# Kernel optimization log

Measured on AMD Instinct MI355X. Metric: run time of the kernel, lower is better.

Reference implementation:

```python
import jax, jax.numpy as jnp
import numpy as np

B, N, C, E = 8, 4096, 128, 131072  # batch, nodes, channels (in==out), edges


def _linear_params(key, fan_in, fan_out):
    kw, kb = jax.random.split(key)
    s = 1.0 / np.sqrt(fan_in).astype(np.float32)
    W = jax.random.uniform(kw, (fan_in, fan_out), jnp.float32, -s, s)
    b = jax.random.uniform(kb, (fan_out,), jnp.float32, -s, s)
    return W, b


def setup_inputs() -> dict:
    key = jax.random.key(0)
    ks = jax.random.split(key, 6)
    x = jax.random.normal(ks[0], (B, N, C), jnp.float32)
    edge_index = jax.random.randint(ks[1], (2, E), 0, N, jnp.int64)
    W0, b0 = _linear_params(ks[2], C, C)        # lin0: in -> out
    W1, b1 = _linear_params(ks[3], 2 * C, C)    # lin1: 2*out -> out
    W2, b2 = _linear_params(ks[4], C, C)        # lin2: out -> out
    Wo, bo = _linear_params(ks[5], C, C)        # output: out -> out
    return {"x": x, "edge_index": edge_index, "W0": W0, "b0": b0,
            "W1": W1, "b1": b1, "W2": W2, "b2": b2, "Wo": Wo, "bo": bo}


def reference(x, edge_index, W0, b0, W1, b1, W2, b2, Wo, bo):
    n = x.shape[1]
    # symmetric 0/1 adjacency (duplicate edges collapse via .set), zero diagonal
    adj = jnp.zeros((n, n), x.dtype)
    adj = adj.at[edge_index[0], edge_index[1]].set(1.0)
    adj = adj.at[edge_index[1], edge_index[0]].set(1.0)
    diag = jnp.arange(n)
    adj = adj.at[diag, diag].set(0.0)
    h = x @ W0 + b0                               # [B, N, C]
    agg = jnp.einsum('ij,bjd->bid', adj, h)       # neighbor aggregation
    cat = jnp.concatenate([x, agg], axis=-1)      # [B, N, 2C]
    out = (cat @ W1 + b1) @ W2 + b2
    out = jax.nn.gelu(out, approximate=False) @ Wo + bo  # torch exact GELU
    return x + out
```

## Files before the change

### kernel.cpp

```cpp
#include <hip/hip_runtime.h>
#include <hip/hip_bf16.h>
#include <math.h>

#define NN 4096
#define BB 8
#define CC 128
#define EE 131072
#define M_ROWS (BB*NN)
#define DEG_CAP 512

typedef __attribute__((ext_vector_type(8))) short short8;
typedef __attribute__((ext_vector_type(4))) float f32x4;

__device__ __forceinline__ float bf2f(unsigned int u){
    union { unsigned int i; float f; } v; v.i = u << 16; return v.f;
}
__device__ __forceinline__ unsigned short f2bf(float f){
    union { float f; unsigned int i; } v; v.f = f;
    unsigned int u = v.i;
    unsigned int r = u + 0x7FFFu + ((u >> 16) & 1u);
    return (unsigned short)(r >> 16);
}

__device__ __forceinline__ int swz(int r, int k2 ){
    return r * 256 + (k2 ^ ((r & 7) << 4));
}

__global__ __launch_bounds__(256) void k_init(uint4* __restrict__ bits4,
                                              const float* __restrict__ x,
                                              unsigned short* __restrict__ xb,
                                              const float* __restrict__ W0, const float* __restrict__ W1,
                                              const float* __restrict__ W2, const float* __restrict__ Wo,
                                              unsigned short* __restrict__ Wt1a, unsigned short* __restrict__ Wt1b,
                                              unsigned short* __restrict__ Wt2,  unsigned short* __restrict__ Wto,
                                              unsigned short* __restrict__ W0bf){
    int bid = blockIdx.x, t = threadIdx.x;
    if (bid < 512){
        bits4[bid * 256 + t] = (uint4){0u, 0u, 0u, 0u};
        return;
    }
    if (bid < 2560){
        size_t e = (size_t)(bid - 512) * 2048 + t * 8;
        float4 lo = *((const float4*)(x + e));
        float4 hi = *((const float4*)(x + e + 4));
        ushort4 w0, w1;
        w0.x = f2bf(lo.x); w0.y = f2bf(lo.y); w0.z = f2bf(lo.z); w0.w = f2bf(lo.w);
        w1.x = f2bf(hi.x); w1.y = f2bf(hi.y); w1.z = f2bf(hi.z); w1.w = f2bf(hi.w);
        *((ushort4*)(xb + e)) = w0;
        *((ushort4*)(xb + e + 4)) = w1;
        return;
    }
    int idx = (bid - 2560) * 256 + t;
    int s = idx >> 14;
    int e = idx & 16383;
    int n = e >> 7, k = e & 127;
    float v; unsigned short* dst;
    switch (s){
        case 0:  v = W1[k*128+n];        dst = Wt1a; break;
        case 1:  v = W1[(128+k)*128+n];  dst = Wt1b; break;
        case 2:  v = W2[k*128+n];        dst = Wt2;  break;
        case 3:  v = Wo[k*128+n];        dst = Wto;  break;
        default: v = W0[n*128+k];        dst = W0bf; break;
    }
    dst[n*128+k] = f2bf(v);
}

__global__ __launch_bounds__(256) void k_scatter(const int* __restrict__ ei,
                                                 unsigned int* __restrict__ bits){
    int e = blockIdx.x * blockDim.x + threadIdx.x;
    if (e < EE){
        int u = ei[e], v = ei[EE + e];
        atomicOr(&bits[u * 128 + (v >> 5)], 1u << (v & 31));
        atomicOr(&bits[v * 128 + (u >> 5)], 1u << (u & 31));
    }
}

__global__ __launch_bounds__(128) void k_csr(const unsigned int* __restrict__ bits,
                                             int* __restrict__ cols, int* __restrict__ deg){
    __shared__ int sc[128];
    int i = blockIdx.x, t = threadIdx.x;
    unsigned int w = bits[i * 128 + t];
    if (t == (i >> 5)) w &= ~(1u << (i & 31));
    int c = __popc(w);
    sc[t] = c; __syncthreads();
    int val = c;
    for (int off = 1; off < 128; off <<= 1){
        int add = (t >= off) ? sc[t - off] : 0;
        __syncthreads();
        val += add; sc[t] = val;
        __syncthreads();
    }
    int total = sc[127];
    int pos = val - c;
    unsigned int ww = w;
    while (ww){
        int b = __ffs(ww) - 1;
        ww &= ww - 1;
        if (pos < DEG_CAP) cols[(size_t)i * DEG_CAP + pos] = t * 32 + b;
        pos++;
    }
    if (t == 0) deg[i] = total < DEG_CAP ? total : DEG_CAP;
}

__device__ __forceinline__ void stage_w(const unsigned short* __restrict__ Wt,
                                        unsigned short* Ws, int t){
    #pragma unroll
    for (int it = 0; it < 8; ++it){
        int g = it * 2048 + t * 8;
        int r = g >> 7, k = g & 127;
        uint4 v = *((const uint4*)(Wt + r * 128 + k));
        *((uint4*)((char*)Ws + swz(r, k * 2))) = v;
    }
}
__device__ __forceinline__ void stage_a_bf16(const unsigned short* __restrict__ src, int blockRow,
                                             unsigned short* As, int t){
    #pragma unroll
    for (int it = 0; it < 4; ++it){
        int g = it * 2048 + t * 8;
        int r = g >> 7, k = g & 127;
        uint4 v = *((const uint4*)(src + (size_t)(blockRow + r) * 128 + k));
        *((uint4*)((char*)As + swz(r, k * 2))) = v;
    }
}
__device__ __forceinline__ void mfma_pass(const unsigned short* As, const unsigned short* Ws,
                                          int wr, int wc, int l15, int lh, f32x4 acc[2][4]){
    #pragma unroll
    for (int ks = 0; ks < 4; ++ks){
        const int kc = ks * 32 + lh * 8;
        short8 af[2], bfv[4];
        #pragma unroll
        for (int m = 0; m < 2; m++){
            int r = wr + m * 16 + l15;
            af[m] = *((const short8*)((const char*)As + swz(r, kc * 2)));
        }
        #pragma unroll
        for (int n = 0; n < 4; n++){
            int r = wc + n * 16 + l15;
            bfv[n] = *((const short8*)((const char*)Ws + swz(r, kc * 2)));
        }
        #pragma unroll
        for (int m = 0; m < 2; m++)
            #pragma unroll
            for (int n = 0; n < 4; n++)
                acc[m][n] = __builtin_amdgcn_mfma_f32_16x16x32_bf16(af[m], bfv[n], acc[m][n], 0, 0, 0);
    }
}

__global__ __launch_bounds__(256) void k_wprod(const unsigned short* __restrict__ W0bf,
                                               const unsigned short* __restrict__ Wt1b,
                                               const float* __restrict__ b0,
                                               const float* __restrict__ W1,
                                               unsigned short* __restrict__ Wtu,
                                               float* __restrict__ c1){
    __shared__ unsigned short As[128*128];
    __shared__ unsigned short Ws[128*128];
    const int t = threadIdx.x;
    stage_w(W0bf, As, t);
    stage_w(Wt1b, Ws, t);
    __syncthreads();
    const int lane = t & 63, w = t >> 6;
    const int wr = w * 32;
    const int l15 = lane & 15, lh = lane >> 4;
    f32x4 acc[2][8];
    #pragma unroll
    for (int m = 0; m < 2; m++) for (int n = 0; n < 8; n++) acc[m][n] = (f32x4)(0.0f);
    #pragma unroll
    for (int ks = 0; ks < 4; ++ks){
        const int kc = ks * 32 + lh * 8;
        short8 af[2], bfv[8];
        #pragma unroll
        for (int m = 0; m < 2; m++){
            int r = wr + m * 16 + l15;
            af[m] = *((const short8*)((const char*)As + swz(r, kc * 2)));
        }
        #pragma unroll
        for (int n = 0; n < 8; n++){
            int r = n * 16 + l15;
            bfv[n] = *((const short8*)((const char*)Ws + swz(r, kc * 2)));
        }
        #pragma unroll
        for (int m = 0; m < 2; m++)
            #pragma unroll
            for (int n = 0; n < 8; n++)
                acc[m][n] = __builtin_amdgcn_mfma_f32_16x16x32_bf16(af[m], bfv[n], acc[m][n], 0, 0, 0);
    }
    #pragma unroll
    for (int m = 0; m < 2; m++){
        #pragma unroll
        for (int rr = 0; rr < 4; rr++){
            int r = wr + m * 16 + lh * 4 + rr;
            #pragma unroll
            for (int n = 0; n < 8; n++){
                int c = n * 16 + l15;
                Wtu[c * 128 + r] = f2bf(acc[m][n][rr]);
            }
        }
    }
    if (t < 128){
        float s = 0.f;
        #pragma unroll 8
        for (int k = 0; k < 128; k++)
            s += b0[k] * W1[(size_t)(128 + k) * 128 + t];
        c1[t] = s;
    }
}

__device__ __forceinline__ void acc8u(uint4 u, float* a){
    a[0] += bf2f(u.x & 0xFFFFu); a[1] += bf2f(u.x >> 16);
    a[2] += bf2f(u.y & 0xFFFFu); a[3] += bf2f(u.y >> 16);
    a[4] += bf2f(u.z & 0xFFFFu); a[5] += bf2f(u.z >> 16);
    a[6] += bf2f(u.w & 0xFFFFu); a[7] += bf2f(u.w >> 16);
}

__global__ __launch_bounds__(256) void k_agg(const unsigned short* __restrict__ h,
                                             const int* __restrict__ cols,
                                             const int* __restrict__ deg,
                                             unsigned short* __restrict__ agg){
    __shared__ int scol[4][DEG_CAP];
    const int t = threadIdx.x;
    const int w = t >> 6, lane = t & 63;
    const int sub = lane >> 4, li = lane & 15;
    const int b = blockIdx.x & 7;
    const int i = ((blockIdx.x >> 3) << 2) + w;
    const int d = deg[i];
    const int* cl = cols + (size_t)i * DEG_CAP;
    for (int q = lane; q < d; q += 64) scol[w][q] = cl[q];

    const unsigned short* hb = h + (size_t)b * (NN*128) + li * 8;
    float a[8];
    #pragma unroll
    for (int c = 0; c < 8; c++) a[c] = 0.f;

    int n = sub;
    for (; n + 4 < d; n += 8){
        int j0 = scol[w][n], j1 = scol[w][n+4];
        uint4 u0 = *((const uint4*)(hb + ((size_t)j0 << 7)));
        uint4 u1 = *((const uint4*)(hb + ((size_t)j1 << 7)));
        acc8u(u0, a); acc8u(u1, a);
    }
    if (n < d){
        uint4 u0 = *((const uint4*)(hb + ((size_t)scol[w][n] << 7)));
        acc8u(u0, a);
    }
    #pragma unroll
    for (int c = 0; c < 8; c++){
        a[c] += __shfl_xor(a[c], 16);
        a[c] += __shfl_xor(a[c], 32);
    }
    if (sub == 0){
        uint4 o;
        o.x = (unsigned)f2bf(a[0]) | ((unsigned)f2bf(a[1]) << 16);
        o.y = (unsigned)f2bf(a[2]) | ((unsigned)f2bf(a[3]) << 16);
        o.z = (unsigned)f2bf(a[4]) | ((unsigned)f2bf(a[5]) << 16);
        o.w = (unsigned)f2bf(a[6]) | ((unsigned)f2bf(a[7]) << 16);
        *((uint4*)(agg + (size_t)b * (NN*128) + ((size_t)i << 7) + li * 8)) = o;
    }
}

__global__ __launch_bounds__(256) void k_mlp(const unsigned short* __restrict__ xb,
                                             const unsigned short* __restrict__ u,
                                             const unsigned short* __restrict__ Wt1a,
                                             const unsigned short* __restrict__ Wtu,
                                             const unsigned short* __restrict__ Wt2,
                                             const unsigned short* __restrict__ Wto,
                                             const float* __restrict__ c1,
                                             const float* __restrict__ b1,
                                             const float* __restrict__ b2,
                                             const float* __restrict__ bo,
                                             const int* __restrict__ deg,
                                             const float* __restrict__ x,
                                             float* __restrict__ out){
    __shared__ unsigned short As[64*128];
    __shared__ unsigned short Ws[128*128];
    const int t = threadIdx.x;
    const int blockRow = blockIdx.x * 64;
    const int lane = t & 63, w = t >> 6;
    const int wr = (w >> 1) * 32, wc = (w & 1) * 64;
    const int l15 = lane & 15, lh = lane >> 4;

    f32x4 acc[2][4];
    #pragma unroll
    for (int m = 0; m < 2; m++) for (int n = 0; n < 4; n++) acc[m][n] = (f32x4)(0.0f);

    stage_a_bf16(xb, blockRow, As, t);
    stage_w(Wt1a, Ws, t);
    __syncthreads();
    mfma_pass(As, Ws, wr, wc, l15, lh, acc);
    __syncthreads();
    stage_a_bf16(u, blockRow, As, t);
    stage_w(Wtu, Ws, t);
    __syncthreads();
    mfma_pass(As, Ws, wr, wc, l15, lh, acc);
    __syncthreads();

    #pragma unroll
    for (int m = 0; m < 2; m++){
        #pragma unroll
        for (int rr = 0; rr < 4; rr++){
            int rl = wr + m * 16 + lh * 4 + rr;
            int node = (blockRow + rl) & (NN - 1);
            float degf = (float)deg[node];
            #pragma unroll
            for (int n = 0; n < 4; n++){
                int col = wc + n * 16 + l15;
                float v = acc[m][n][rr] + b1[col] + degf * c1[col];
                *((unsigned short*)((char*)As + swz(rl, col * 2))) = f2bf(v);
            }
        }
    }
    stage_w(Wt2, Ws, t);
    __syncthreads();

    f32x4 acc2[2][4];
    #pragma unroll
    for (int m = 0; m < 2; m++) for (int n = 0; n < 4; n++) acc2[m][n] = (f32x4)(0.0f);
    mfma_pass(As, Ws, wr, wc, l15, lh, acc2);
    __syncthreads();

    #pragma unroll
    for (int m = 0; m < 2; m++){
        #pragma unroll
        for (int rr = 0; rr < 4; rr++){
            int rl = wr + m * 16 + lh * 4 + rr;
            #pragma unroll
            for (int n = 0; n < 4; n++){
                int col = wc + n * 16 + l15;
                float v = acc2[m][n][rr] + b2[col];
                v = 0.5f * v * (1.0f + erff(v * 0.70710678118f));
                *((unsigned short*)((char*)As + swz(rl, col * 2))) = f2bf(v);
            }
        }
    }
    stage_w(Wto, Ws, t);
    __syncthreads();

    f32x4 acc3[2][4];
    #pragma unroll
    for (int m = 0; m < 2; m++) for (int n = 0; n < 4; n++) acc3[m][n] = (f32x4)(0.0f);
    mfma_pass(As, Ws, wr, wc, l15, lh, acc3);

    #pragma unroll
    for (int m = 0; m < 2; m++){
        #pragma unroll
        for (int rr = 0; rr < 4; rr++){
            int row = blockRow + wr + m * 16 + lh * 4 + rr;
            #pragma unroll
            for (int n = 0; n < 4; n++){
                int col = wc + n * 16 + l15;
                float v = acc3[m][n][rr] + bo[col] + x[(size_t)row * 128 + col];
                out[(size_t)row * 128 + col] = v;
            }
        }
    }
}

extern "C" void kernel_launch(void* const* d_in, const int* in_sizes, int n_in,
                              void* d_out, int out_size, void* d_ws, size_t ws_size,
                              hipStream_t stream) {
    const float* x  = (const float*)d_in[0];
    const int*   ei = (const int*)d_in[1];
    const float* W0 = (const float*)d_in[2];
    const float* b0 = (const float*)d_in[3];
    const float* W1 = (const float*)d_in[4];
    const float* b1 = (const float*)d_in[5];
    const float* W2 = (const float*)d_in[6];
    const float* b2 = (const float*)d_in[7];
    const float* Wo = (const float*)d_in[8];
    const float* bo = (const float*)d_in[9];
    float* out = (float*)d_out;

    char* ws = (char*)d_ws;
    unsigned int* bits   = (unsigned int*)(ws + 0);
    int*   cols          = (int*)(ws + 2097152);
    int*   deg           = (int*)(ws + 10485760);
    unsigned short* xb   = (unsigned short*)(ws + 10502144);
    unsigned short* ubuf = (unsigned short*)(ws + 18890752);
    unsigned short* Wt1a = (unsigned short*)(ws + 27279360);
    unsigned short* Wt1b = (unsigned short*)(ws + 27279360 + 32768);
    unsigned short* Wt2  = (unsigned short*)(ws + 27279360 + 65536);
    unsigned short* Wto  = (unsigned short*)(ws + 27279360 + 98304);
    unsigned short* W0bf = (unsigned short*)(ws + 27279360 + 131072);
    unsigned short* Wtu  = (unsigned short*)(ws + 27279360 + 163840);
    float* c1            = (float*)(ws + 27279360 + 196608);

    k_init<<<2880, 256, 0, stream>>>((uint4*)bits, x, xb, W0, W1, W2, Wo,
                                     Wt1a, Wt1b, Wt2, Wto, W0bf);
    k_scatter<<<EE / 256, 256, 0, stream>>>(ei, bits);
    k_csr<<<NN, 128, 0, stream>>>(bits, cols, deg);
    k_wprod<<<1, 256, 0, stream>>>(W0bf, Wt1b, b0, W1, Wtu, c1);
    k_agg<<<BB * (NN / 4), 256, 0, stream>>>(xb, cols, deg, ubuf);
    k_mlp<<<M_ROWS / 64, 256, 0, stream>>>(xb, ubuf, Wt1a, Wtu, Wt2, Wto,
                                           c1, b1, b2, bo, deg, x, out);
}
```

Before: 77.13 us.

## Fuse weight-product into scatter kernel, shrink CSR cols to u16, residual from bf16 tile

Result: no change. 77.10 us (-0.0%).

```diff
diff --git a/kernel.cpp b/kernel.cpp
--- a/kernel.cpp
+++ b/kernel.cpp
@@ -65,18 +65,120 @@
     dst[n*128+k] = f2bf(v);
 }
 
+__device__ __forceinline__ void stage_w(const unsigned short* __restrict__ Wt,
+                                        unsigned short* Ws, int t){
+    #pragma unroll
+    for (int it = 0; it < 8; ++it){
+        int g = it * 2048 + t * 8;
+        int r = g >> 7, k = g & 127;
+        uint4 v = *((const uint4*)(Wt + r * 128 + k));
+        *((uint4*)((char*)Ws + swz(r, k * 2))) = v;
+    }
+}
+__device__ __forceinline__ void stage_a_bf16(const unsigned short* __restrict__ src, int blockRow,
+                                             unsigned short* As, int t){
+    #pragma unroll
+    for (int it = 0; it < 4; ++it){
+        int g = it * 2048 + t * 8;
+        int r = g >> 7, k = g & 127;
+        uint4 v = *((const uint4*)(src + (size_t)(blockRow + r) * 128 + k));
+        *((uint4*)((char*)As + swz(r, k * 2))) = v;
+    }
+}
+__device__ __forceinline__ void mfma_pass(const unsigned short* As, const unsigned short* Ws,
+                                          int wr, int wc, int l15, int lh, f32x4 acc[2][4]){
+    #pragma unroll
+    for (int ks = 0; ks < 4; ++ks){
+        const int kc = ks * 32 + lh * 8;
+        short8 af[2], bfv[4];
+        #pragma unroll
+        for (int m = 0; m < 2; m++){
+            int r = wr + m * 16 + l15;
+            af[m] = *((const short8*)((const char*)As + swz(r, kc * 2)));
+        }
+        #pragma unroll
+        for (int n = 0; n < 4; n++){
+            int r = wc + n * 16 + l15;
+            bfv[n] = *((const short8*)((const char*)Ws + swz(r, kc * 2)));
+        }
+        #pragma unroll
+        for (int m = 0; m < 2; m++)
+            #pragma unroll
+            for (int n = 0; n < 4; n++)
+                acc[m][n] = __builtin_amdgcn_mfma_f32_16x16x32_bf16(af[m], bfv[n], acc[m][n], 0, 0, 0);
+    }
+}
+
 __global__ __launch_bounds__(256) void k_scatter(const int* __restrict__ ei,
-                                                 unsigned int* __restrict__ bits){
-    int e = blockIdx.x * blockDim.x + threadIdx.x;
-    if (e < EE){
+                                                 unsigned int* __restrict__ bits,
+                                                 const unsigned short* __restrict__ W0bf,
+                                                 const unsigned short* __restrict__ Wt1b,
+                                                 const float* __restrict__ b0,
+                                                 const float* __restrict__ W1,
+                                                 unsigned short* __restrict__ Wtu,
+                                                 float* __restrict__ c1){
+    const int bid = blockIdx.x, t = threadIdx.x;
+    if (bid < 512){
+        int e = bid * 256 + t;
         int u = ei[e], v = ei[EE + e];
         atomicOr(&bits[u * 128 + (v >> 5)], 1u << (v & 31));
         atomicOr(&bits[v * 128 + (u >> 5)], 1u << (u & 31));
+        return;
+    }
+    __shared__ unsigned short As[128*128];
+    __shared__ unsigned short Ws[128*128];
+    stage_w(W0bf, As, t);
+    stage_w(Wt1b, Ws, t);
+    __syncthreads();
+    const int lane = t & 63, w = t >> 6;
+    const int wr = w * 32;
+    const int l15 = lane & 15, lh = lane >> 4;
+    f32x4 acc[2][8];
+    #pragma unroll
+    for (int m = 0; m < 2; m++) for (int n = 0; n < 8; n++) acc[m][n] = (f32x4)(0.0f);
+    #pragma unroll
+    for (int ks = 0; ks < 4; ++ks){
+        const int kc = ks * 32 + lh * 8;
+        short8 af[2], bfv[8];
+        #pragma unroll
+        for (int m = 0; m < 2; m++){
+            int r = wr + m * 16 + l15;
+            af[m] = *((const short8*)((const char*)As + swz(r, kc * 2)));
+        }
+        #pragma unroll
+        for (int n = 0; n < 8; n++){
+            int r = n * 16 + l15;
+            bfv[n] = *((const short8*)((const char*)Ws + swz(r, kc * 2)));
+        }
+        #pragma unroll
+        for (int m = 0; m < 2; m++)
+            #pragma unroll
+            for (int n = 0; n < 8; n++)
+                acc[m][n] = __builtin_amdgcn_mfma_f32_16x16x32_bf16(af[m], bfv[n], acc[m][n], 0, 0, 0);
+    }
+    #pragma unroll
+    for (int m = 0; m < 2; m++){
+        #pragma unroll
+        for (int rr = 0; rr < 4; rr++){
+            int r = wr + m * 16 + lh * 4 + rr;
+            #pragma unroll
+            for (int n = 0; n < 8; n++){
+                int c = n * 16 + l15;
+                Wtu[c * 128 + r] = f2bf(acc[m][n][rr]);
+            }
+        }
+    }
+    if (t < 128){
+        float s = 0.f;
+        #pragma unroll 8
+        for (int k = 0; k < 128; k++)
+            s += b0[k] * W1[(size_t)(128 + k) * 128 + t];
+        c1[t] = s;
     }
 }
 
 __global__ __launch_bounds__(128) void k_csr(const unsigned int* __restrict__ bits,
-                                             int* __restrict__ cols, int* __restrict__ deg){
+                                             unsigned short* __restrict__ cols, int* __restrict__ deg){
     __shared__ int sc[128];
     int i = blockIdx.x, t = threadIdx.x;
     unsigned int w = bits[i * 128 + t];
@@ -96,113 +198,10 @@
     while (ww){
         int b = __ffs(ww) - 1;
         ww &= ww - 1;
-        if (pos < DEG_CAP) cols[(size_t)i * DEG_CAP + pos] = t * 32 + b;
+        if (pos < DEG_CAP) cols[(size_t)i * DEG_CAP + pos] = (unsigned short)(t * 32 + b);
         pos++;
     }
     if (t == 0) deg[i] = total < DEG_CAP ? total : DEG_CAP;
-}
-
-__device__ __forceinline__ void stage_w(const unsigned short* __restrict__ Wt,
-                                        unsigned short* Ws, int t){
-    #pragma unroll
-    for (int it = 0; it < 8; ++it){
-        int g = it * 2048 + t * 8;
-        int r = g >> 7, k = g & 127;
-        uint4 v = *((const uint4*)(Wt + r * 128 + k));
-        *((uint4*)((char*)Ws + swz(r, k * 2))) = v;
-    }
-}
-__device__ __forceinline__ void stage_a_bf16(const unsigned short* __restrict__ src, int blockRow,
-                                             unsigned short* As, int t){
-    #pragma unroll
-    for (int it = 0; it < 4; ++it){
-        int g = it * 2048 + t * 8;
-        int r = g >> 7, k = g & 127;
-        uint4 v = *((const uint4*)(src + (size_t)(blockRow + r) * 128 + k));
-        *((uint4*)((char*)As + swz(r, k * 2))) = v;
-    }
-}
-__device__ __forceinline__ void mfma_pass(const unsigned short* As, const unsigned short* Ws,
-                                          int wr, int wc, int l15, int lh, f32x4 acc[2][4]){
-    #pragma unroll
-    for (int ks = 0; ks < 4; ++ks){
-        const int kc = ks * 32 + lh * 8;
-        short8 af[2], bfv[4];
-        #pragma unroll
-        for (int m = 0; m < 2; m++){
-            int r = wr + m * 16 + l15;
-            af[m] = *((const short8*)((const char*)As + swz(r, kc * 2)));
-        }
-        #pragma unroll
-        for (int n = 0; n < 4; n++){
-            int r = wc + n * 16 + l15;
-            bfv[n] = *((const short8*)((const char*)Ws + swz(r, kc * 2)));
-        }
-        #pragma unroll
-        for (int m = 0; m < 2; m++)
-            #pragma unroll
-            for (int n = 0; n < 4; n++)
-                acc[m][n] = __builtin_amdgcn_mfma_f32_16x16x32_bf16(af[m], bfv[n], acc[m][n], 0, 0, 0);
-    }
-}
-
-__global__ __launch_bounds__(256) void k_wprod(const unsigned short* __restrict__ W0bf,
-                                               const unsigned short* __restrict__ Wt1b,
-                                               const float* __restrict__ b0,
-                                               const float* __restrict__ W1,
-                                               unsigned short* __restrict__ Wtu,
-                                               float* __restrict__ c1){
-    __shared__ unsigned short As[128*128];
-    __shared__ unsigned short Ws[128*128];
-    const int t = threadIdx.x;
-    stage_w(W0bf, As, t);
-    stage_w(Wt1b, Ws, t);
-    __syncthreads();
-    const int lane = t & 63, w = t >> 6;
-    const int wr = w * 32;
-    const int l15 = lane & 15, lh = lane >> 4;
-    f32x4 acc[2][8];
-    #pragma unroll
-    for (int m = 0; m < 2; m++) for (int n = 0; n < 8; n++) acc[m][n] = (f32x4)(0.0f);
-    #pragma unroll
-    for (int ks = 0; ks < 4; ++ks){
-        const int kc = ks * 32 + lh * 8;
-        short8 af[2], bfv[8];
-        #pragma unroll
-        for (int m = 0; m < 2; m++){
-            int r = wr + m * 16 + l15;
-            af[m] = *((const short8*)((const char*)As + swz(r, kc * 2)));
-        }
-        #pragma unroll
-        for (int n = 0; n < 8; n++){
-            int r = n * 16 + l15;
-            bfv[n] = *((const short8*)((const char*)Ws + swz(r, kc * 2)));
-        }
-        #pragma unroll
-        for (int m = 0; m < 2; m++)
-            #pragma unroll
-            for (int n = 0; n < 8; n++)
-                acc[m][n] = __builtin_amdgcn_mfma_f32_16x16x32_bf16(af[m], bfv[n], acc[m][n], 0, 0, 0);
-    }
-    #pragma unroll
-    for (int m = 0; m < 2; m++){
-        #pragma unroll
-        for (int rr = 0; rr < 4; rr++){
-            int r = wr + m * 16 + lh * 4 + rr;
-            #pragma unroll
-            for (int n = 0; n < 8; n++){
-                int c = n * 16 + l15;
-                Wtu[c * 128 + r] = f2bf(acc[m][n][rr]);
-            }
-        }
-    }
-    if (t < 128){
-        float s = 0.f;
-        #pragma unroll 8
-        for (int k = 0; k < 128; k++)
-            s += b0[k] * W1[(size_t)(128 + k) * 128 + t];
-        c1[t] = s;
-    }
 }
 
 __device__ __forceinline__ void acc8u(uint4 u, float* a){
@@ -213,17 +212,17 @@
 }
 
 __global__ __launch_bounds__(256) void k_agg(const unsigned short* __restrict__ h,
-                                             const int* __restrict__ cols,
+                                             const unsigned short* __restrict__ cols,
                                              const int* __restrict__ deg,
                                              unsigned short* __restrict__ agg){
-    __shared__ int scol[4][DEG_CAP];
+    __shared__ unsigned short scol[4][DEG_CAP];
     const int t = threadIdx.x;
     const int w = t >> 6, lane = t & 63;
     const int sub = lane >> 4, li = lane & 15;
     const int b = blockIdx.x & 7;
     const int i = ((blockIdx.x >> 3) << 2) + w;
     const int d = deg[i];
-    const int* cl = cols + (size_t)i * DEG_CAP;
+    const unsigned short* cl = cols + (size_t)i * DEG_CAP;
     for (int q = lane; q < d; q += 64) scol[w][q] = cl[q];
 
     const unsigned short* hb = h + (size_t)b * (NN*128) + li * 8;
@@ -268,7 +267,6 @@
                                              const float* __restrict__ b2,
                                              const float* __restrict__ bo,
                                              const int* __restrict__ deg,
-                                             const float* __restrict__ x,
                                              float* __restrict__ out){
     __shared__ unsigned short As[64*128];
     __shared__ unsigned short Ws[128*128];
@@ -286,7 +284,23 @@
     stage_w(Wt1a, Ws, t);
     __syncthreads();
     mfma_pass(As, Ws, wr, wc, l15, lh, acc);
-    __syncthreads();
+
+    f32x4 acc3[2][4];
+    #pragma unroll
+    for (int m = 0; m < 2; m++){
+        #pragma unroll
+        for (int rr = 0; rr < 4; rr++){
+            int rl = wr + m * 16 + lh * 4 + rr;
+            #pragma unroll
+            for (int n = 0; n < 4; n++){
+                int col = wc + n * 16 + l15;
+                unsigned int us = *((const unsigned short*)((const char*)As + swz(rl, col * 2)));
+                acc3[m][n][rr] = bf2f(us) + bo[col];
+            }
+        }
+    }
+    __syncthreads();
+
     stage_a_bf16(u, blockRow, As, t);
     stage_w(Wtu, Ws, t);
     __syncthreads();
@@ -334,9 +348,6 @@
     stage_w(Wto, Ws, t);
     __syncthreads();
 
-    f32x4 acc3[2][4];
-    #pragma unroll
-    for (int m = 0; m < 2; m++) for (int n = 0; n < 4; n++) acc3[m][n] = (f32x4)(0.0f);
     mfma_pass(As, Ws, wr, wc, l15, lh, acc3);
 
     #pragma unroll
@@ -347,8 +358,7 @@
             #pragma unroll
             for (int n = 0; n < 4; n++){
                 int col = wc + n * 16 + l15;
-                float v = acc3[m][n][rr] + bo[col] + x[(size_t)row * 128 + col];
-                out[(size_t)row * 128 + col] = v;
+                out[(size_t)row * 128 + col] = acc3[m][n][rr];
             }
         }
     }
@@ -370,25 +380,24 @@
     float* out = (float*)d_out;
 
     char* ws = (char*)d_ws;
-    unsigned int* bits   = (unsigned int*)(ws + 0);
-    int*   cols          = (int*)(ws + 2097152);
-    int*   deg           = (int*)(ws + 10485760);
-    unsigned short* xb   = (unsigned short*)(ws + 10502144);
-    unsigned short* ubuf = (unsigned short*)(ws + 18890752);
-    unsigned short* Wt1a = (unsigned short*)(ws + 27279360);
-    unsigned short* Wt1b = (unsigned short*)(ws + 27279360 + 32768);
-    unsigned short* Wt2  = (unsigned short*)(ws + 27279360 + 65536);
-    unsigned short* Wto  = (unsigned short*)(ws + 27279360 + 98304);
-    unsigned short* W0bf = (unsigned short*)(ws + 27279360 + 131072);
-    unsigned short* Wtu  = (unsigned short*)(ws + 27279360 + 163840);
-    float* c1            = (float*)(ws + 27279360 + 196608);
+    unsigned int* bits    = (unsigned int*)(ws + 0);
+    unsigned short* cols  = (unsigned short*)(ws + 2097152);
+    int*   deg            = (int*)(ws + 6291456);
+    unsigned short* xb    = (unsigned short*)(ws + 6307840);
+    unsigned short* ubuf  = (unsigned short*)(ws + 14696448);
+    unsigned short* Wt1a  = (unsigned short*)(ws + 23085056);
+    unsigned short* Wt1b  = (unsigned short*)(ws + 23085056 + 32768);
+    unsigned short* Wt2   = (unsigned short*)(ws + 23085056 + 65536);
+    unsigned short* Wto   = (unsigned short*)(ws + 23085056 + 98304);
+    unsigned short* W0bf  = (unsigned short*)(ws + 23085056 + 131072);
+    unsigned short* Wtu   = (unsigned short*)(ws + 23085056 + 163840);
+    float* c1             = (float*)(ws + 23085056 + 196608);
 
     k_init<<<2880, 256, 0, stream>>>((uint4*)bits, x, xb, W0, W1, W2, Wo,
                                      Wt1a, Wt1b, Wt2, Wto, W0bf);
-    k_scatter<<<EE / 256, 256, 0, stream>>>(ei, bits);
+    k_scatter<<<513, 256, 0, stream>>>(ei, bits, W0bf, Wt1b, b0, W1, Wtu, c1);
     k_csr<<<NN, 128, 0, stream>>>(bits, cols, deg);
-    k_wprod<<<1, 256, 0, stream>>>(W0bf, Wt1b, b0, W1, Wtu, c1);
     k_agg<<<BB * (NN / 4), 256, 0, stream>>>(xb, cols, deg, ubuf);
     k_mlp<<<M_ROWS / 64, 256, 0, stream>>>(xb, ubuf, Wt1a, Wtu, Wt2, Wto,
-                                           c1, b1, b2, bo, deg, x, out);
-}
+                                           c1, b1, b2, bo, deg, out);
+}
```
